# Optimization experiments

Hardware: AMD Instinct MI355X
Metric: run time of the kernel (lower is better)

Reference implementation:

```python
import jax, jax.numpy as jnp
import numpy as np

NBINS = 256  # skimage threshold_otsu default
RGB_W = np.array([0.2989, 0.5870, 0.1140], dtype=np.float32)  # tf.image.rgb_to_grayscale weights


def setup_inputs() -> dict:
    key = jax.random.key(0)
    inputs = jax.random.uniform(key, (16, 1024, 1024, 3), dtype=jnp.float32)
    return {"inputs": inputs}


def _otsu_threshold(x_flat):
    # Histogram over [min, max] with NBINS bins (skimage semantics: one
    # global threshold over the whole array passed to threshold_otsu).
    mn = x_flat.min()
    mx = x_flat.max()
    width = (mx - mn) / NBINS
    idx = jnp.clip(((x_flat - mn) / width).astype(jnp.int32), 0, NBINS - 1)
    counts = jnp.zeros((NBINS,), jnp.float32).at[idx].add(1.0)
    centers = mn + width * (jnp.arange(NBINS, dtype=jnp.float32) + 0.5)

    # class-separation (between-class variance) per candidate split
    w1 = jnp.cumsum(counts)                      # weight of class 1 (<= t)
    w2 = jnp.cumsum(counts[::-1])[::-1]          # weight of class 2 (> t)
    s1 = jnp.cumsum(counts * centers)
    s2 = jnp.cumsum((counts * centers)[::-1])[::-1]
    m1 = s1 / jnp.maximum(w1, 1.0)
    m2 = s2 / jnp.maximum(w2, 1.0)
    var12 = w1[:-1] * w2[1:] * (m1[:-1] - m2[1:]) ** 2
    return centers[jnp.argmax(var12)]


def reference(inputs):
    # rgb -> grayscale (tf.image.rgb_to_grayscale weights), keep channel dim
    gray = jnp.einsum('bhwc,c->bhw', inputs[..., :3], jnp.asarray(RGB_W))[..., None]
    thresh = _otsu_threshold(gray.ravel())  # single global threshold over the whole batch
    return jnp.where(gray > thresh, 1.0, 0.0).astype(jnp.float32)
```

## Files before the change

kernel.cpp:

```cpp
#include <hip/hip_runtime.h>


static constexpr float W0 = 0.2989f;
static constexpr float W1 = 0.5870f;
static constexpr float W2 = 0.1140f;

__device__ __forceinline__ float gray_of(float r, float g, float b) {
    return __fadd_rn(__fadd_rn(__fmul_rn(r, W0), __fmul_rn(g, W1)), __fmul_rn(b, W2));
}

__global__ __launch_bounds__(256) void k_gray(
        const float4* __restrict__ in4, float4* __restrict__ gray4,
        float* __restrict__ pmin, float* __restrict__ pmax, int ntiles) {
    __shared__ float4 sv[768];
    int t = threadIdx.x;
    float lmin = __uint_as_float(0x7f800000u);
    float lmax = -lmin;
    for (int tile = blockIdx.x; tile < ntiles; tile += gridDim.x) {
        const float4* src = in4 + (size_t)tile * 768;
        float4 v0 = src[t];
        float4 v1 = src[t + 256];
        float4 v2 = src[t + 512];
        __syncthreads();
        sv[t] = v0; sv[t + 256] = v1; sv[t + 512] = v2;
        __syncthreads();
        float4 a = sv[3 * t + 0];
        float4 b = sv[3 * t + 1];
        float4 c = sv[3 * t + 2];
        float g0 = gray_of(a.x, a.y, a.z);
        float g1 = gray_of(a.w, b.x, b.y);
        float g2 = gray_of(b.z, b.w, c.x);
        float g3 = gray_of(c.y, c.z, c.w);
        float4 o; o.x = g0; o.y = g1; o.z = g2; o.w = g3;
        gray4[(size_t)tile * 256 + t] = o;
        lmin = fminf(lmin, fminf(fminf(g0, g1), fminf(g2, g3)));
        lmax = fmaxf(lmax, fmaxf(fmaxf(g0, g1), fmaxf(g2, g3)));
    }
    #pragma unroll
    for (int off = 32; off > 0; off >>= 1) {
        lmin = fminf(lmin, __shfl_down(lmin, off));
        lmax = fmaxf(lmax, __shfl_down(lmax, off));
    }
    __shared__ float smin[4], smax[4];
    int wave = t >> 6, lane = t & 63;
    if (lane == 0) { smin[wave] = lmin; smax[wave] = lmax; }
    __syncthreads();
    if (t == 0) {
        pmin[blockIdx.x] = fminf(fminf(smin[0], smin[1]), fminf(smin[2], smin[3]));
        pmax[blockIdx.x] = fmaxf(fmaxf(smax[0], smax[1]), fmaxf(smax[2], smax[3]));
    }
}

__global__ __launch_bounds__(256) void k_reduce(
        const float* __restrict__ pmin, const float* __restrict__ pmax,
        float* __restrict__ minmax, int n) {
    int t = threadIdx.x;
    float lmin = __uint_as_float(0x7f800000u);
    float lmax = -lmin;
    for (int i = t; i < n; i += blockDim.x) {
        lmin = fminf(lmin, pmin[i]);
        lmax = fmaxf(lmax, pmax[i]);
    }
    #pragma unroll
    for (int off = 32; off > 0; off >>= 1) {
        lmin = fminf(lmin, __shfl_down(lmin, off));
        lmax = fmaxf(lmax, __shfl_down(lmax, off));
    }
    __shared__ float smin[4], smax[4];
    int wave = t >> 6, lane = t & 63;
    if (lane == 0) { smin[wave] = lmin; smax[wave] = lmax; }
    __syncthreads();
    if (t == 0) {
        minmax[0] = fminf(fminf(smin[0], smin[1]), fminf(smin[2], smin[3]));
        minmax[1] = fmaxf(fmaxf(smax[0], smax[1]), fmaxf(smax[2], smax[3]));
    }
}

__global__ __launch_bounds__(256) void k_hist(
        const float4* __restrict__ gray4, const float* __restrict__ minmax,
        unsigned* __restrict__ hist_part, int npix4) {
    __shared__ unsigned lh[4 * 256];
    for (int j = threadIdx.x; j < 4 * 256; j += 256) lh[j] = 0u;
    __syncthreads();
    float mn = minmax[0];
    float mx = minmax[1];
    float width = __fdiv_rn(__fsub_rn(mx, mn), 256.0f);
    unsigned* myh = &lh[(threadIdx.x >> 6) << 8];
    int stride = gridDim.x * blockDim.x;
    for (int i = blockIdx.x * blockDim.x + threadIdx.x; i < npix4; i += stride) {
        float4 g = gray4[i];
        int i0 = (int)__fdiv_rn(__fsub_rn(g.x, mn), width);
        int i1 = (int)__fdiv_rn(__fsub_rn(g.y, mn), width);
        int i2 = (int)__fdiv_rn(__fsub_rn(g.z, mn), width);
        int i3 = (int)__fdiv_rn(__fsub_rn(g.w, mn), width);
        i0 = min(max(i0, 0), 255);
        i1 = min(max(i1, 0), 255);
        i2 = min(max(i2, 0), 255);
        i3 = min(max(i3, 0), 255);
        atomicAdd(&myh[i0], 1u);
        atomicAdd(&myh[i1], 1u);
        atomicAdd(&myh[i2], 1u);
        atomicAdd(&myh[i3], 1u);
    }
    __syncthreads();
    int b = threadIdx.x;
    hist_part[(size_t)blockIdx.x * 256 + b] = lh[b] + lh[256 + b] + lh[512 + b] + lh[768 + b];
}

__global__ __launch_bounds__(1024) void k_otsu(
        const unsigned* __restrict__ hist_part, int nparts,
        const float* __restrict__ minmax, float* __restrict__ thresh) {
    __shared__ unsigned csum[4 * 256];
    __shared__ float counts[256], centers[256], tt[256];
    __shared__ float w1[256], s1[256], w2[256], s2[256], vv[256];
    int t = threadIdx.x;
    int b = t & 255, q = t >> 8;
    unsigned acc = 0;
    for (int k = q; k < nparts; k += 4)
        acc += hist_part[(size_t)k * 256 + b];
    csum[q * 256 + b] = acc;
    __syncthreads();
    if (t < 256) {
        unsigned c = csum[t] + csum[256 + t] + csum[512 + t] + csum[768 + t];
        float mn = minmax[0];
        float mx = minmax[1];
        float width = __fdiv_rn(__fsub_rn(mx, mn), 256.0f);
        counts[t] = (float)c;
        centers[t] = __fadd_rn(mn, __fmul_rn(width, __fadd_rn((float)t, 0.5f)));
        tt[t] = __fmul_rn(counts[t], centers[t]);
    }
    __syncthreads();
    if (t == 0) {
        float aw = 0.0f, as = 0.0f;
        #pragma unroll 16
        for (int i = 0; i < 256; ++i) {
            aw = __fadd_rn(aw, counts[i]); w1[i] = aw;
            as = __fadd_rn(as, tt[i]);     s1[i] = as;
        }
        aw = 0.0f; as = 0.0f;
        #pragma unroll 16
        for (int i = 255; i >= 0; --i) {
            aw = __fadd_rn(aw, counts[i]); w2[i] = aw;
            as = __fadd_rn(as, tt[i]);     s2[i] = as;
        }
    }
    __syncthreads();
    if (t < 255) {
        float m1 = __fdiv_rn(s1[t],     fmaxf(w1[t],     1.0f));
        float m2 = __fdiv_rn(s2[t + 1], fmaxf(w2[t + 1], 1.0f));
        float d  = __fsub_rn(m1, m2);
        vv[t] = __fmul_rn(__fmul_rn(w1[t], w2[t + 1]), __fmul_rn(d, d));
    }
    __syncthreads();
    if (t == 0) {
        float best = -1.0f; int bi = 0;
        #pragma unroll 16
        for (int i = 0; i < 255; ++i) {
            float v = vv[i];
            if (v > best) { best = v; bi = i; }
        }
        *thresh = centers[bi];
    }
}

__global__ __launch_bounds__(256) void k_bin(
        float4* __restrict__ g4, const float* __restrict__ thresh, int npix4) {
    int i = blockIdx.x * blockDim.x + threadIdx.x;
    float th = *thresh;
    if (i < npix4) {
        float4 g = g4[i];
        float4 o;
        o.x = g.x > th ? 1.0f : 0.0f;
        o.y = g.y > th ? 1.0f : 0.0f;
        o.z = g.z > th ? 1.0f : 0.0f;
        o.w = g.w > th ? 1.0f : 0.0f;
        g4[i] = o;
    }
}

extern "C" void kernel_launch(void* const* d_in, const int* in_sizes, int n_in,
                              void* d_out, int out_size, void* d_ws, size_t ws_size,
                              hipStream_t stream) {
    const float4* in4 = (const float4*)d_in[0];
    float4* gray4 = (float4*)d_out;

    int npix = in_sizes[0] / 3;
    int npix4 = npix / 4;
    int ntiles = npix / 1024;
    int grayBlocks = ntiles < 2048 ? ntiles : 2048;

    float* pmin = (float*)d_ws;
    float* pmax = pmin + grayBlocks;
    float* minmax = pmax + grayBlocks;
    float* thresh = minmax + 2;
    unsigned* hist_part = (unsigned*)(thresh + 1);
    size_t used = (size_t)(2 * grayBlocks + 3) * sizeof(float);
    int histBlocks = 1024;
    if (ws_size < used + (size_t)histBlocks * 256 * sizeof(unsigned)) {
        size_t avail = (ws_size > used) ? (ws_size - used) : 0;
        histBlocks = (int)(avail / (256 * sizeof(unsigned)));
        if (histBlocks > 1024) histBlocks = 1024;
        if (histBlocks < 1) histBlocks = 1;
    }

    k_gray<<<grayBlocks, 256, 0, stream>>>(in4, gray4, pmin, pmax, ntiles);
    k_reduce<<<1, 256, 0, stream>>>(pmin, pmax, minmax, grayBlocks);
    k_hist<<<histBlocks, 256, 0, stream>>>((const float4*)d_out, minmax, hist_part, npix4);
    k_otsu<<<1, 1024, 0, stream>>>(hist_part, histBlocks, minmax, thresh);
    k_bin<<<(npix4 + 255) / 256, 256, 0, stream>>>(gray4, thresh, npix4);
}
```

Baseline: 387.8 us.

## Fuse gray, reduce, histogram, Otsu and binarize into one cooperative kernel

Replaces the five-kernel pipeline with a single persistent cooperative kernel of 1024 blocks that uses grid-wide syncs between the grayscale/min-max, histogram, Otsu threshold and binarize phases. The goal is to remove the per-kernel launch gaps and the tail idle time between dependent stages. In exchange it pays for three grid barriers, and the threshold computation now runs serially in block 0 while every other block waits. If the cooperative launch fails, the old kernels run instead, but that fallback sizes the workspace for 1024 partials while k_gray still writes 2048, so pmin and pmax overlap there.

Result: slower. 714.0 us (+84.1%).

```diff
diff --git a/kernel.cpp b/kernel.cpp
--- a/kernel.cpp
+++ b/kernel.cpp
@@ -1,4 +1,7 @@
 #include <hip/hip_runtime.h>
+#include <hip/hip_cooperative_groups.h>
+
+namespace cg = cooperative_groups;
 
 
 static constexpr float W0 = 0.2989f;
@@ -7,6 +10,167 @@
 
 __device__ __forceinline__ float gray_of(float r, float g, float b) {
     return __fadd_rn(__fadd_rn(__fmul_rn(r, W0), __fmul_rn(g, W1)), __fmul_rn(b, W2));
+}
+
+__device__ __forceinline__ void wave_minmax(float& lmin, float& lmax) {
+    #pragma unroll
+    for (int off = 32; off > 0; off >>= 1) {
+        lmin = fminf(lmin, __shfl_down(lmin, off));
+        lmax = fmaxf(lmax, __shfl_down(lmax, off));
+    }
+}
+
+__global__ __launch_bounds__(256, 4) void k_fused(
+        const float4* __restrict__ in4, float4* __restrict__ gray4,
+        float* __restrict__ pmin, float* __restrict__ pmax,
+        unsigned* __restrict__ hist_part, float* __restrict__ thresh,
+        int ntiles, int npix4) {
+    cg::grid_group grid = cg::this_grid();
+    __shared__ __align__(16) char smraw[12288];
+    float4*   stage   = (float4*)smraw;
+    unsigned* lh      = (unsigned*)smraw;
+    float*    counts  = (float*)smraw;
+    float*    centers = counts + 256;
+    float*    tt      = counts + 512;
+    float*    w1      = counts + 768;
+    float*    s1      = counts + 1024;
+    float*    w2      = counts + 1280;
+    float*    s2      = counts + 1536;
+    float*    vv      = counts + 1792;
+    __shared__ float sredA[4], sredB[4];
+    __shared__ float s_mn, s_mx;
+
+    const int t = threadIdx.x;
+    const int bid = blockIdx.x;
+    const int nb = gridDim.x;
+
+    float lmin = __uint_as_float(0x7f800000u);
+    float lmax = -lmin;
+    for (int tile = bid; tile < ntiles; tile += nb) {
+        const float4* src = in4 + (size_t)tile * 768;
+        float4 v0 = src[t];
+        float4 v1 = src[t + 256];
+        float4 v2 = src[t + 512];
+        __syncthreads();
+        stage[t] = v0; stage[t + 256] = v1; stage[t + 512] = v2;
+        __syncthreads();
+        float4 a = stage[3 * t + 0];
+        float4 b = stage[3 * t + 1];
+        float4 c = stage[3 * t + 2];
+        float g0 = gray_of(a.x, a.y, a.z);
+        float g1 = gray_of(a.w, b.x, b.y);
+        float g2 = gray_of(b.z, b.w, c.x);
+        float g3 = gray_of(c.y, c.z, c.w);
+        float4 o; o.x = g0; o.y = g1; o.z = g2; o.w = g3;
+        gray4[(size_t)tile * 256 + t] = o;
+        lmin = fminf(lmin, fminf(fminf(g0, g1), fminf(g2, g3)));
+        lmax = fmaxf(lmax, fmaxf(fmaxf(g0, g1), fmaxf(g2, g3)));
+    }
+    wave_minmax(lmin, lmax);
+    if ((t & 63) == 0) { sredA[t >> 6] = lmin; sredB[t >> 6] = lmax; }
+    __syncthreads();
+    if (t == 0) {
+        pmin[bid] = fminf(fminf(sredA[0], sredA[1]), fminf(sredA[2], sredA[3]));
+        pmax[bid] = fmaxf(fmaxf(sredB[0], sredB[1]), fmaxf(sredB[2], sredB[3]));
+    }
+    grid.sync();
+
+    lmin = __uint_as_float(0x7f800000u);
+    lmax = -lmin;
+    for (int i = t; i < nb; i += 256) {
+        lmin = fminf(lmin, pmin[i]);
+        lmax = fmaxf(lmax, pmax[i]);
+    }
+    wave_minmax(lmin, lmax);
+    __syncthreads();
+    if ((t & 63) == 0) { sredA[t >> 6] = lmin; sredB[t >> 6] = lmax; }
+    __syncthreads();
+    if (t == 0) {
+        s_mn = fminf(fminf(sredA[0], sredA[1]), fminf(sredA[2], sredA[3]));
+        s_mx = fmaxf(fmaxf(sredB[0], sredB[1]), fmaxf(sredB[2], sredB[3]));
+    }
+    __syncthreads();
+    const float mn = s_mn;
+    const float mx = s_mx;
+    const float width = __fdiv_rn(__fsub_rn(mx, mn), 256.0f);
+
+    for (int j = t; j < 1024; j += 256) lh[j] = 0u;
+    __syncthreads();
+    unsigned* myh = &lh[(t >> 6) << 8];
+    for (int i = bid * 256 + t; i < npix4; i += nb * 256) {
+        float4 g = gray4[i];
+        int i0 = (int)__fdiv_rn(__fsub_rn(g.x, mn), width);
+        int i1 = (int)__fdiv_rn(__fsub_rn(g.y, mn), width);
+        int i2 = (int)__fdiv_rn(__fsub_rn(g.z, mn), width);
+        int i3 = (int)__fdiv_rn(__fsub_rn(g.w, mn), width);
+        i0 = min(max(i0, 0), 255);
+        i1 = min(max(i1, 0), 255);
+        i2 = min(max(i2, 0), 255);
+        i3 = min(max(i3, 0), 255);
+        atomicAdd(&myh[i0], 1u);
+        atomicAdd(&myh[i1], 1u);
+        atomicAdd(&myh[i2], 1u);
+        atomicAdd(&myh[i3], 1u);
+    }
+    __syncthreads();
+    unsigned hsum = lh[t] + lh[256 + t] + lh[512 + t] + lh[768 + t];
+    hist_part[(size_t)bid * 256 + t] = hsum;
+    grid.sync();
+
+    if (bid == 0) {
+        unsigned c = 0;
+        #pragma unroll 8
+        for (int k = 0; k < nb; ++k)
+            c += hist_part[(size_t)k * 256 + t];
+        __syncthreads();
+        counts[t] = (float)c;
+        centers[t] = __fadd_rn(mn, __fmul_rn(width, __fadd_rn((float)t, 0.5f)));
+        tt[t] = __fmul_rn(counts[t], centers[t]);
+        __syncthreads();
+        if (t == 0) {
+            float aw = 0.0f, as = 0.0f;
+            #pragma unroll 16
+            for (int i = 0; i < 256; ++i) {
+                aw = __fadd_rn(aw, counts[i]); w1[i] = aw;
+                as = __fadd_rn(as, tt[i]);     s1[i] = as;
+            }
+            aw = 0.0f; as = 0.0f;
+            #pragma unroll 16
+            for (int i = 255; i >= 0; --i) {
+                aw = __fadd_rn(aw, counts[i]); w2[i] = aw;
+                as = __fadd_rn(as, tt[i]);     s2[i] = as;
+            }
+        }
+        __syncthreads();
+        if (t < 255) {
+            float m1 = __fdiv_rn(s1[t],     fmaxf(w1[t],     1.0f));
+            float m2 = __fdiv_rn(s2[t + 1], fmaxf(w2[t + 1], 1.0f));
+            float d  = __fsub_rn(m1, m2);
+            vv[t] = __fmul_rn(__fmul_rn(w1[t], w2[t + 1]), __fmul_rn(d, d));
+        }
+        __syncthreads();
+        if (t == 0) {
+            float best = -1.0f; int bi = 0;
+            #pragma unroll 16
+            for (int i = 0; i < 255; ++i) {
+                float v = vv[i];
+                if (v > best) { best = v; bi = i; }
+            }
+            thresh[0] = centers[bi];
+        }
+    }
+    grid.sync();
+
+    const float th = thresh[0];
+    for (int i = bid * 256 + t; i < npix4; i += nb * 256) {
+        float4 g = gray4[i];
+        float4 o;
+        o.x = g.x > th ? 1.0f : 0.0f;
+        o.y = g.y > th ? 1.0f : 0.0f;
+        o.z = g.z > th ? 1.0f : 0.0f;
+        o.w = g.w > th ? 1.0f : 0.0f;
+        gray4[i] = o;
+    }
 }
 
 __global__ __launch_bounds__(256) void k_gray(
@@ -36,14 +200,9 @@
         lmin = fminf(lmin, fminf(fminf(g0, g1), fminf(g2, g3)));
         lmax = fmaxf(lmax, fmaxf(fmaxf(g0, g1), fmaxf(g2, g3)));
     }
-    #pragma unroll
-    for (int off = 32; off > 0; off >>= 1) {
-        lmin = fminf(lmin, __shfl_down(lmin, off));
-        lmax = fmaxf(lmax, __shfl_down(lmax, off));
-    }
+    wave_minmax(lmin, lmax);
     __shared__ float smin[4], smax[4];
-    int wave = t >> 6, lane = t & 63;
-    if (lane == 0) { smin[wave] = lmin; smax[wave] = lmax; }
+    if ((t & 63) == 0) { smin[t >> 6] = lmin; smax[t >> 6] = lmax; }
     __syncthreads();
     if (t == 0) {
         pmin[blockIdx.x] = fminf(fminf(smin[0], smin[1]), fminf(smin[2], smin[3]));
@@ -57,18 +216,13 @@
     int t = threadIdx.x;
     float lmin = __uint_as_float(0x7f800000u);
     float lmax = -lmin;
-    for (int i = t; i < n; i += blockDim.x) {
+    for (int i = t; i < n; i += 256) {
         lmin = fminf(lmin, pmin[i]);
         lmax = fmaxf(lmax, pmax[i]);
     }
-    #pragma unroll
-    for (int off = 32; off > 0; off >>= 1) {
-        lmin = fminf(lmin, __shfl_down(lmin, off));
-        lmax = fmaxf(lmax, __shfl_down(lmax, off));
-    }
+    wave_minmax(lmin, lmax);
     __shared__ float smin[4], smax[4];
-    int wave = t >> 6, lane = t & 63;
-    if (lane == 0) { smin[wave] = lmin; smax[wave] = lmax; }
+    if ((t & 63) == 0) { smin[t >> 6] = lmin; smax[t >> 6] = lmax; }
     __syncthreads();
     if (t == 0) {
         minmax[0] = fminf(fminf(smin[0], smin[1]), fminf(smin[2], smin[3]));
@@ -79,8 +233,8 @@
 __global__ __launch_bounds__(256) void k_hist(
         const float4* __restrict__ gray4, const float* __restrict__ minmax,
         unsigned* __restrict__ hist_part, int npix4) {
-    __shared__ unsigned lh[4 * 256];
-    for (int j = threadIdx.x; j < 4 * 256; j += 256) lh[j] = 0u;
+    __shared__ unsigned lh[1024];
+    for (int j = threadIdx.x; j < 1024; j += 256) lh[j] = 0u;
     __syncthreads();
     float mn = minmax[0];
     float mx = minmax[1];
@@ -110,7 +264,7 @@
 __global__ __launch_bounds__(1024) void k_otsu(
         const unsigned* __restrict__ hist_part, int nparts,
         const float* __restrict__ minmax, float* __restrict__ thresh) {
-    __shared__ unsigned csum[4 * 256];
+    __shared__ unsigned csum[1024];
     __shared__ float counts[256], centers[256], tt[256];
     __shared__ float w1[256], s1[256], w2[256], s2[256], vv[256];
     int t = threadIdx.x;
@@ -132,13 +286,11 @@
     __syncthreads();
     if (t == 0) {
         float aw = 0.0f, as = 0.0f;
-        #pragma unroll 16
         for (int i = 0; i < 256; ++i) {
             aw = __fadd_rn(aw, counts[i]); w1[i] = aw;
             as = __fadd_rn(as, tt[i]);     s1[i] = as;
         }
         aw = 0.0f; as = 0.0f;
-        #pragma unroll 16
         for (int i = 255; i >= 0; --i) {
             aw = __fadd_rn(aw, counts[i]); w2[i] = aw;
             as = __fadd_rn(as, tt[i]);     s2[i] = as;
@@ -154,7 +306,6 @@
     __syncthreads();
     if (t == 0) {
         float best = -1.0f; int bi = 0;
-        #pragma unroll 16
         for (int i = 0; i < 255; ++i) {
             float v = vv[i];
             if (v > best) { best = v; bi = i; }
@@ -187,25 +338,24 @@
     int npix = in_sizes[0] / 3;
     int npix4 = npix / 4;
     int ntiles = npix / 1024;
-    int grayBlocks = ntiles < 2048 ? ntiles : 2048;
-
+
+    const int NB = 1024;
     float* pmin = (float*)d_ws;
-    float* pmax = pmin + grayBlocks;
-    float* minmax = pmax + grayBlocks;
+    float* pmax = pmin + NB;
+    float* minmax = pmax + NB;
     float* thresh = minmax + 2;
     unsigned* hist_part = (unsigned*)(thresh + 1);
-    size_t used = (size_t)(2 * grayBlocks + 3) * sizeof(float);
-    int histBlocks = 1024;
-    if (ws_size < used + (size_t)histBlocks * 256 * sizeof(unsigned)) {
-        size_t avail = (ws_size > used) ? (ws_size - used) : 0;
-        histBlocks = (int)(avail / (256 * sizeof(unsigned)));
-        if (histBlocks > 1024) histBlocks = 1024;
-        if (histBlocks < 1) histBlocks = 1;
-    }
-
-    k_gray<<<grayBlocks, 256, 0, stream>>>(in4, gray4, pmin, pmax, ntiles);
-    k_reduce<<<1, 256, 0, stream>>>(pmin, pmax, minmax, grayBlocks);
-    k_hist<<<histBlocks, 256, 0, stream>>>((const float4*)d_out, minmax, hist_part, npix4);
-    k_otsu<<<1, 1024, 0, stream>>>(hist_part, histBlocks, minmax, thresh);
-    k_bin<<<(npix4 + 255) / 256, 256, 0, stream>>>(gray4, thresh, npix4);
-}
+
+    void* args[] = { (void*)&in4, (void*)&gray4, (void*)&pmin, (void*)&pmax,
+                     (void*)&hist_part, (void*)&thresh, (void*)&ntiles, (void*)&npix4 };
+    hipError_t err = hipLaunchCooperativeKernel((const void*)k_fused,
+                                                dim3(NB), dim3(256), args, 0, stream);
+    if (err != hipSuccess) {
+        (void)hipGetLastError();
+        k_gray<<<2048, 256, 0, stream>>>(in4, gray4, pmin, pmax, ntiles);
+        k_reduce<<<1, 256, 0, stream>>>(pmin, pmax, minmax, 2048);
+        k_hist<<<NB, 256, 0, stream>>>((const float4*)d_out, minmax, hist_part, npix4);
+        k_otsu<<<1, 1024, 0, stream>>>(hist_part, NB, minmax, thresh);
+        k_bin<<<(npix4 + 255) / 256, 256, 0, stream>>>(gray4, thresh, npix4);
+    }
+}
```

## Fold min/max reduce and Otsu scan into histogram and binarize kernels

Applied to the files above, without the earlier changes.

Removes the single-block reduce and Otsu kernels. Every histogram block and every binarize block now reduces the per-block min/max partials on its own, and every binarize block recomputes the Otsu threshold from the histogram partials before a grid-stride binarize pass. This cuts the launch count from five to three and removes two serial single-block kernels, and it also changes the gray, histogram and binarize grid sizes. In exchange, every binarize block redundantly reads all 512x256 histogram partials and runs the serial scans. The workspace-size guard is dropped, and the gray grid now uses a fixed 4096 blocks.

Result: faster. 371.9 us (-4.1%).

```diff
diff --git a/kernel.cpp b/kernel.cpp
--- a/kernel.cpp
+++ b/kernel.cpp
@@ -5,8 +5,39 @@
 static constexpr float W1 = 0.5870f;
 static constexpr float W2 = 0.1140f;
 
+static constexpr int GRAY_BLOCKS = 4096;
+static constexpr int HIST_BLOCKS = 512;
+static constexpr int BIN_BLOCKS  = 1024;
+
 __device__ __forceinline__ float gray_of(float r, float g, float b) {
     return __fadd_rn(__fadd_rn(__fmul_rn(r, W0), __fmul_rn(g, W1)), __fmul_rn(b, W2));
+}
+
+__device__ __forceinline__ void wave_minmax(float& lmin, float& lmax) {
+    #pragma unroll
+    for (int off = 32; off > 0; off >>= 1) {
+        lmin = fminf(lmin, __shfl_down(lmin, off));
+        lmax = fmaxf(lmax, __shfl_down(lmax, off));
+    }
+}
+
+__device__ __forceinline__ void reduce_partials(
+        const float* __restrict__ pmin, const float* __restrict__ pmax,
+        int n, float& out_mn, float& out_mx) {
+    __shared__ float smin[4], smax[4];
+    int t = threadIdx.x;
+    float lmin = __uint_as_float(0x7f800000u);
+    float lmax = -lmin;
+    for (int i = t; i < n; i += 256) {
+        lmin = fminf(lmin, pmin[i]);
+        lmax = fmaxf(lmax, pmax[i]);
+    }
+    wave_minmax(lmin, lmax);
+    if ((t & 63) == 0) { smin[t >> 6] = lmin; smax[t >> 6] = lmax; }
+    __syncthreads();
+    out_mn = fminf(fminf(smin[0], smin[1]), fminf(smin[2], smin[3]));
+    out_mx = fmaxf(fmaxf(smax[0], smax[1]), fmaxf(smax[2], smax[3]));
+    __syncthreads();
 }
 
 __global__ __launch_bounds__(256) void k_gray(
@@ -36,14 +67,9 @@
         lmin = fminf(lmin, fminf(fminf(g0, g1), fminf(g2, g3)));
         lmax = fmaxf(lmax, fmaxf(fmaxf(g0, g1), fmaxf(g2, g3)));
     }
-    #pragma unroll
-    for (int off = 32; off > 0; off >>= 1) {
-        lmin = fminf(lmin, __shfl_down(lmin, off));
-        lmax = fmaxf(lmax, __shfl_down(lmax, off));
-    }
+    wave_minmax(lmin, lmax);
     __shared__ float smin[4], smax[4];
-    int wave = t >> 6, lane = t & 63;
-    if (lane == 0) { smin[wave] = lmin; smax[wave] = lmax; }
+    if ((t & 63) == 0) { smin[t >> 6] = lmin; smax[t >> 6] = lmax; }
     __syncthreads();
     if (t == 0) {
         pmin[blockIdx.x] = fminf(fminf(smin[0], smin[1]), fminf(smin[2], smin[3]));
@@ -51,43 +77,20 @@
     }
 }
 
-__global__ __launch_bounds__(256) void k_reduce(
+__global__ __launch_bounds__(256) void k_hist(
+        const float4* __restrict__ gray4,
         const float* __restrict__ pmin, const float* __restrict__ pmax,
-        float* __restrict__ minmax, int n) {
-    int t = threadIdx.x;
-    float lmin = __uint_as_float(0x7f800000u);
-    float lmax = -lmin;
-    for (int i = t; i < n; i += blockDim.x) {
-        lmin = fminf(lmin, pmin[i]);
-        lmax = fmaxf(lmax, pmax[i]);
-    }
-    #pragma unroll
-    for (int off = 32; off > 0; off >>= 1) {
-        lmin = fminf(lmin, __shfl_down(lmin, off));
-        lmax = fmaxf(lmax, __shfl_down(lmax, off));
-    }
-    __shared__ float smin[4], smax[4];
-    int wave = t >> 6, lane = t & 63;
-    if (lane == 0) { smin[wave] = lmin; smax[wave] = lmax; }
+        unsigned* __restrict__ hist_part, int npix4) {
+    float mn, mx;
+    reduce_partials(pmin, pmax, GRAY_BLOCKS, mn, mx);
+    float width = __fdiv_rn(__fsub_rn(mx, mn), 256.0f);
+
+    __shared__ unsigned lh[1024];
+    for (int j = threadIdx.x; j < 1024; j += 256) lh[j] = 0u;
     __syncthreads();
-    if (t == 0) {
-        minmax[0] = fminf(fminf(smin[0], smin[1]), fminf(smin[2], smin[3]));
-        minmax[1] = fmaxf(fmaxf(smax[0], smax[1]), fmaxf(smax[2], smax[3]));
-    }
-}
-
-__global__ __launch_bounds__(256) void k_hist(
-        const float4* __restrict__ gray4, const float* __restrict__ minmax,
-        unsigned* __restrict__ hist_part, int npix4) {
-    __shared__ unsigned lh[4 * 256];
-    for (int j = threadIdx.x; j < 4 * 256; j += 256) lh[j] = 0u;
-    __syncthreads();
-    float mn = minmax[0];
-    float mx = minmax[1];
-    float width = __fdiv_rn(__fsub_rn(mx, mn), 256.0f);
     unsigned* myh = &lh[(threadIdx.x >> 6) << 8];
-    int stride = gridDim.x * blockDim.x;
-    for (int i = blockIdx.x * blockDim.x + threadIdx.x; i < npix4; i += stride) {
+    int stride = gridDim.x * 256;
+    for (int i = blockIdx.x * 256 + threadIdx.x; i < npix4; i += stride) {
         float4 g = gray4[i];
         int i0 = (int)__fdiv_rn(__fsub_rn(g.x, mn), width);
         int i1 = (int)__fdiv_rn(__fsub_rn(g.y, mn), width);
@@ -104,31 +107,30 @@
     }
     __syncthreads();
     int b = threadIdx.x;
-    hist_part[(size_t)blockIdx.x * 256 + b] = lh[b] + lh[256 + b] + lh[512 + b] + lh[768 + b];
+    hist_part[(size_t)blockIdx.x * 256 + b] =
+        lh[b] + lh[256 + b] + lh[512 + b] + lh[768 + b];
 }
 
-__global__ __launch_bounds__(1024) void k_otsu(
-        const unsigned* __restrict__ hist_part, int nparts,
-        const float* __restrict__ minmax, float* __restrict__ thresh) {
-    __shared__ unsigned csum[4 * 256];
+__global__ __launch_bounds__(256) void k_bin(
+        float4* __restrict__ g4,
+        const float* __restrict__ pmin, const float* __restrict__ pmax,
+        const unsigned* __restrict__ hist_part, int npix4) {
+    float mn, mx;
+    reduce_partials(pmin, pmax, GRAY_BLOCKS, mn, mx);
+    float width = __fdiv_rn(__fsub_rn(mx, mn), 256.0f);
+
     __shared__ float counts[256], centers[256], tt[256];
     __shared__ float w1[256], s1[256], w2[256], s2[256], vv[256];
+    __shared__ float s_th;
     int t = threadIdx.x;
-    int b = t & 255, q = t >> 8;
-    unsigned acc = 0;
-    for (int k = q; k < nparts; k += 4)
-        acc += hist_part[(size_t)k * 256 + b];
-    csum[q * 256 + b] = acc;
-    __syncthreads();
-    if (t < 256) {
-        unsigned c = csum[t] + csum[256 + t] + csum[512 + t] + csum[768 + t];
-        float mn = minmax[0];
-        float mx = minmax[1];
-        float width = __fdiv_rn(__fsub_rn(mx, mn), 256.0f);
-        counts[t] = (float)c;
-        centers[t] = __fadd_rn(mn, __fmul_rn(width, __fadd_rn((float)t, 0.5f)));
-        tt[t] = __fmul_rn(counts[t], centers[t]);
-    }
+
+    unsigned c = 0;
+    #pragma unroll 8
+    for (int k = 0; k < HIST_BLOCKS; ++k)
+        c += hist_part[(size_t)k * 256 + t];
+    counts[t] = (float)c;
+    centers[t] = __fadd_rn(mn, __fmul_rn(width, __fadd_rn((float)t, 0.5f)));
+    tt[t] = __fmul_rn(counts[t], centers[t]);
     __syncthreads();
     if (t == 0) {
         float aw = 0.0f, as = 0.0f;
@@ -159,15 +161,13 @@
             float v = vv[i];
             if (v > best) { best = v; bi = i; }
         }
-        *thresh = centers[bi];
+        s_th = centers[bi];
     }
-}
+    __syncthreads();
+    const float th = s_th;
 
-__global__ __launch_bounds__(256) void k_bin(
-        float4* __restrict__ g4, const float* __restrict__ thresh, int npix4) {
-    int i = blockIdx.x * blockDim.x + threadIdx.x;
-    float th = *thresh;
-    if (i < npix4) {
+    int stride = gridDim.x * 256;
+    for (int i = blockIdx.x * 256 + t; i < npix4; i += stride) {
         float4 g = g4[i];
         float4 o;
         o.x = g.x > th ? 1.0f : 0.0f;
@@ -187,25 +187,13 @@
     int npix = in_sizes[0] / 3;
     int npix4 = npix / 4;
     int ntiles = npix / 1024;
-    int grayBlocks = ntiles < 2048 ? ntiles : 2048;
 
     float* pmin = (float*)d_ws;
-    float* pmax = pmin + grayBlocks;
-    float* minmax = pmax + grayBlocks;
-    float* thresh = minmax + 2;
-    unsigned* hist_part = (unsigned*)(thresh + 1);
-    size_t used = (size_t)(2 * grayBlocks + 3) * sizeof(float);
-    int histBlocks = 1024;
-    if (ws_size < used + (size_t)histBlocks * 256 * sizeof(unsigned)) {
-        size_t avail = (ws_size > used) ? (ws_size - used) : 0;
-        histBlocks = (int)(avail / (256 * sizeof(unsigned)));
-        if (histBlocks > 1024) histBlocks = 1024;
-        if (histBlocks < 1) histBlocks = 1;
-    }
+    float* pmax = pmin + GRAY_BLOCKS;
+    unsigned* hist_part = (unsigned*)(pmax + GRAY_BLOCKS);
 
-    k_gray<<<grayBlocks, 256, 0, stream>>>(in4, gray4, pmin, pmax, ntiles);
-    k_reduce<<<1, 256, 0, stream>>>(pmin, pmax, minmax, grayBlocks);
-    k_hist<<<histBlocks, 256, 0, stream>>>((const float4*)d_out, minmax, hist_part, npix4);
-    k_otsu<<<1, 1024, 0, stream>>>(hist_part, histBlocks, minmax, thresh);
-    k_bin<<<(npix4 + 255) / 256, 256, 0, stream>>>(gray4, thresh, npix4);
+    k_gray<<<GRAY_BLOCKS, 256, 0, stream>>>(in4, gray4, pmin, pmax, ntiles);
+    k_hist<<<HIST_BLOCKS, 256, 0, stream>>>((const float4*)d_out, pmin, pmax,
+                                            hist_part, npix4);
+    k_bin<<<BIN_BLOCKS, 256, 0, stream>>>(gray4, pmin, pmax, hist_part, npix4);
 }
```
